# Kernel tuning notes

Measured on AMD Instinct MI355X. Metric: run time of the kernel, lower is better.

## Reference

```python
import jax, jax.numpy as jnp
import numpy as np

B, C, H, W = 8, 512, 96, 96
CQ = 64  # in_places // scale
EPS = 1e-06


def setup_inputs() -> dict:
    key = jax.random.key(0)
    ks = jax.random.split(key, 4)
    x = jax.random.normal(ks[0], (B, C, H, W), dtype=jnp.float32)
    wq = jax.random.normal(ks[1], (CQ, C), dtype=jnp.float32) * (1.0 / np.sqrt(C))
    wk = jax.random.normal(ks[2], (CQ, C), dtype=jnp.float32) * (1.0 / np.sqrt(C))
    wv = jax.random.normal(ks[3], (C, C), dtype=jnp.float32) * (1.0 / np.sqrt(C))
    bq = jnp.zeros((CQ,), jnp.float32)
    bk = jnp.zeros((CQ,), jnp.float32)
    bv = jnp.zeros((C,), jnp.float32)
    gamma = jnp.ones((1,), jnp.float32)
    return {"x": x, "wq": wq, "bq": bq, "wk": wk, "bk": bk, "wv": wv, "bv": bv, "gamma": gamma}


def reference(x, wq, bq, wk, bk, wv, bv, gamma):
    b, c, h, w = x.shape
    n = h * w
    xf = x.reshape(b, c, n)  # [b, c, n]
    # 1x1 convs == per-position channel GEMMs
    Q = jnp.einsum('oc,bcn->bon', wq, xf) + bq[None, :, None]  # [b, cq, n]
    K = jnp.einsum('oc,bcn->bon', wk, xf) + bk[None, :, None]  # [b, cq, n]
    V = jnp.einsum('oc,bcn->bon', wv, xf) + bv[None, :, None]  # [b, c, n]
    # L2 normalize over channel dim (dim=-2), matching torch l2_norm (no eps)
    Q = Q / jnp.linalg.norm(Q, axis=1, keepdims=True)
    K = K / jnp.linalg.norm(K, axis=1, keepdims=True)
    Qt = jnp.transpose(Q, (0, 2, 1))  # [b, n, cq]
    # tailor_sum = 1 / (N + Q . (sum_n K + eps))
    k_sum = K.sum(axis=-1) + EPS  # [b, cq]
    tailor = 1.0 / (n + jnp.einsum('bnm,bm->bn', Qt, k_sum))  # [b, n]
    v_sum = V.sum(axis=-1)  # [b, c]
    matrix = jnp.einsum('bmn,bcn->bmc', K, V)  # [b, cq, c]
    matrix_sum = v_sum[:, :, None] + jnp.einsum('bnm,bmc->bcn', Qt, matrix)  # [b, c, n]
    weight_value = matrix_sum * tailor[:, None, :]  # [b, c, n]
    return x + gamma[0] * weight_value.reshape(b, c, h, w)
```

## Files before the change

### kernel.cpp

```cpp
#include <hip/hip_runtime.h>

#define NB 8
#define NC 512
#define NQ 64
#define NN 9216
#define FEPS 1e-6f

typedef __attribute__((ext_vector_type(8))) short s16x8;
typedef __attribute__((ext_vector_type(4))) float f32x4;

static const size_t OFF_Q    = 0;
static const size_t OFF_KT   = OFF_Q + (size_t)NB * NQ * NN;
static const size_t OFF_KSUM = OFF_KT + (size_t)NB * NQ * NN;
static const size_t OFF_XSUM = OFF_KSUM + (size_t)NB * NQ;
static const size_t OFF_M1   = OFF_XSUM + (size_t)NB * NC;
static const size_t OFF_M2   = OFF_M1 + (size_t)NB * NQ * NC;
static const size_t OFF_VSUM = OFF_M2 + (size_t)NB * NQ * NC;
static const size_t OFF_WB   = OFF_VSUM + (size_t)NB * NC;

__device__ __forceinline__ void load_lds16(const void* g, void* l) {
    __builtin_amdgcn_global_load_lds((const __attribute__((address_space(1))) void*)g,
                                     (__attribute__((address_space(3))) void*)l, 16, 0, 0);
}

__device__ __forceinline__ unsigned cvt_pk_bf16(float lo, float hi) {
    unsigned r;
    asm("v_cvt_pk_bf16_f32 %0, %1, %2" : "=v"(r) : "v"(lo), "v"(hi));
    return r;
}

__device__ __forceinline__ unsigned short f2bf(float f) {
    union { float f; unsigned u; } a; a.f = f;
    unsigned r = a.u + 0x7FFFu + ((a.u >> 16) & 1u);
    return (unsigned short)(r >> 16);
}

__global__ void prep_w_kernel(const float* __restrict__ wq, const float* __restrict__ wk,
                              unsigned short* __restrict__ Wb) {
    const int idx = blockIdx.x * 256 + threadIdx.x;
#pragma unroll
    for (int k = 0; k < 4; ++k) {
        const int f4 = idx + k * 4096;
        const float* src = (f4 < 8192) ? wq : wk;
        const float4 v = *(const float4*)&src[(size_t)(f4 & 8191) * 4];
        uint2 u;
        u.x = cvt_pk_bf16(v.x, v.y);
        u.y = cvt_pk_bf16(v.z, v.w);
        *(uint2*)&Wb[(size_t)f4 * 4] = u;
    }
}

__launch_bounds__(256, 3)
__global__ void qk_mfma_kernel(const float* __restrict__ x,
                               const unsigned short* __restrict__ Wb,
                               const float* __restrict__ bq, const float* __restrict__ bk,
                               float* __restrict__ Qt, unsigned short* __restrict__ Ktb,
                               float* __restrict__ ksum) {
    __shared__ __align__(16) unsigned short WX[12672];
    __shared__ float ssqL[4][64];
    unsigned short* Ws = WX;
    unsigned short* Xs = WX + 8192;
    const int t = threadIdx.x;
    const int w = t >> 6, lane = t & 63;
    const int g = lane >> 4, i16 = lane & 15;
    const int b = blockIdx.y;
    const int n0 = blockIdx.x * 64;
    const int srow = (w << 3) + (lane >> 3);
    const int sslot = lane & 7;

    f32x4 acc[2][4];
#pragma unroll
    for (int rt = 0; rt < 2; ++rt)
#pragma unroll
        for (int ct = 0; ct < 4; ++ct) acc[rt][ct] = {0.f, 0.f, 0.f, 0.f};

#pragma unroll 1
    for (int kc = 0; kc < NC; kc += 64) {
#pragma unroll
        for (int q = 0; q < 4; ++q) {
            const int row = q * 32 + srow;
            load_lds16(Wb + (size_t)row * NC + kc + ((sslot ^ (row & 7)) << 3),
                       Ws + (q * 32 + (w << 3)) * 64);
        }
#pragma unroll
        for (int r = 0; r < 2; ++r) {
            const int idx = r * 256 + t;
            const int cp = idx >> 4;
            const int p4 = (idx & 15) << 2;
            const float* xp = &x[((size_t)b * NC + kc + 2 * cp) * NN + n0 + p4];
            const float4 v0 = *(const float4*)xp;
            const float4 v1 = *(const float4*)(xp + NN);
            const float* f0 = (const float*)&v0;
            const float* f1 = (const float*)&v1;
#pragma unroll
            for (int j = 0; j < 4; ++j) {
                const int pos = p4 + j;
                const unsigned u = cvt_pk_bf16(f0[j], f1[j]);
                *(unsigned*)&Xs[pos * 64 + ((2 * cp) ^ ((pos & 7) << 3))] = u;
            }
        }
        __syncthreads();
#pragma unroll
        for (int ks = 0; ks < 2; ++ks) {
            s16x8 af[2], bfr[4];
#pragma unroll
            for (int rt = 0; rt < 2; ++rt) {
                const int row = (w << 5) + (rt << 4) + i16;
                af[rt] = *(const s16x8*)&Ws[row * 64 + (((ks << 5) + (g << 3)) ^ ((row & 7) << 3))];
            }
#pragma unroll
            for (int ct = 0; ct < 4; ++ct) {
                const int row = (ct << 4) + i16;
                bfr[ct] = *(const s16x8*)&Xs[row * 64 + (((ks << 5) + (g << 3)) ^ ((row & 7) << 3))];
            }
#pragma unroll
            for (int rt = 0; rt < 2; ++rt)
#pragma unroll
                for (int ct = 0; ct < 4; ++ct)
                    acc[rt][ct] = __builtin_amdgcn_mfma_f32_16x16x32_bf16(af[rt], bfr[ct], acc[rt][ct], 0, 0, 0);
        }
        __syncthreads();
    }

    const bool isK = (w >= 2);
    const int obase = (w & 1) * 32;
    const float* bias = isK ? bk : bq;
    float bv[2][4];
#pragma unroll
    for (int rt = 0; rt < 2; ++rt)
#pragma unroll
        for (int reg = 0; reg < 4; ++reg)
            bv[rt][reg] = bias[obase + rt * 16 + 4 * g + reg];
#pragma unroll
    for (int rt = 0; rt < 2; ++rt)
#pragma unroll
        for (int ct = 0; ct < 4; ++ct)
#pragma unroll
            for (int reg = 0; reg < 4; ++reg) acc[rt][ct][reg] += bv[rt][reg];

    float sq[4];
#pragma unroll
    for (int ct = 0; ct < 4; ++ct) {
        float s = 0.f;
#pragma unroll
        for (int rt = 0; rt < 2; ++rt)
#pragma unroll
            for (int reg = 0; reg < 4; ++reg) s += acc[rt][ct][reg] * acc[rt][ct][reg];
        s += __shfl_xor(s, 16, 64);
        s += __shfl_xor(s, 32, 64);
        sq[ct] = s;
    }
    ssqL[w][lane] = sq[g];
    __syncthreads();
    const int pairw = (w >> 1) << 1;
    float inv[4];
#pragma unroll
    for (int ct = 0; ct < 4; ++ct) {
        const int p = ct * 16 + i16;
        inv[ct] = rsqrtf(ssqL[pairw][p] + ssqL[pairw + 1][p]);
    }
#pragma unroll
    for (int rt = 0; rt < 2; ++rt)
#pragma unroll
        for (int ct = 0; ct < 4; ++ct)
#pragma unroll
            for (int reg = 0; reg < 4; ++reg) acc[rt][ct][reg] *= inv[ct];

    float* epQ = (float*)WX;
    unsigned short* epK = WX + 8320;
    if (!isK) {
#pragma unroll
        for (int rt = 0; rt < 2; ++rt)
#pragma unroll
            for (int ct = 0; ct < 4; ++ct)
#pragma unroll
                for (int reg = 0; reg < 4; ++reg)
                    epQ[(ct * 16 + i16) * 65 + (w * 32 + rt * 16 + 4 * g + reg)] = acc[rt][ct][reg];
    } else {
#pragma unroll
        for (int rt = 0; rt < 2; ++rt)
#pragma unroll
            for (int reg = 0; reg < 4; ++reg) {
                float s = acc[rt][0][reg] + acc[rt][1][reg] + acc[rt][2][reg] + acc[rt][3][reg];
                s += __shfl_xor(s, 1, 64);
                s += __shfl_xor(s, 2, 64);
                s += __shfl_xor(s, 4, 64);
                s += __shfl_xor(s, 8, 64);
                if (i16 == 0) atomicAdd(&ksum[b * NQ + obase + rt * 16 + 4 * g + reg], s);
            }
#pragma unroll
        for (int rt = 0; rt < 2; ++rt)
#pragma unroll
            for (int ct = 0; ct < 4; ++ct)
#pragma unroll
                for (int reg = 0; reg < 4; ++reg)
                    epK[(obase + rt * 16 + 4 * g + reg) * 68 + ct * 16 + i16] = f2bf(acc[rt][ct][reg]);
    }
    __syncthreads();
#pragma unroll
    for (int r = 0; r < 4; ++r) {
        const int idx = r * 256 + t;
        const int o = idx >> 4, p4 = (idx & 15) * 4;
        float4 v;
        v.x = epQ[(p4 + 0) * 65 + o];
        v.y = epQ[(p4 + 1) * 65 + o];
        v.z = epQ[(p4 + 2) * 65 + o];
        v.w = epQ[(p4 + 3) * 65 + o];
        *(float4*)&Qt[((size_t)b * NQ + o) * NN + n0 + p4] = v;
    }
#pragma unroll
    for (int r = 0; r < 2; ++r) {
        const int idx = r * 256 + t;
        const int o = idx >> 3, s8 = (idx & 7) * 8;
        uint4 pk;
        unsigned short* up = (unsigned short*)&pk;
#pragma unroll
        for (int j = 0; j < 8; ++j) up[j] = epK[o * 68 + s8 + j];
        *(uint4*)&Ktb[((size_t)b * NQ + o) * NN + n0 + s8] = pk;
    }
}

__launch_bounds__(256, 4)
__global__ void kxt_mfma_kernel(const float* __restrict__ x, const unsigned short* __restrict__ Ktb,
                                float* __restrict__ mat1, float* __restrict__ xsum) {
    __shared__ __align__(16) unsigned short Ks[64 * 64];
    __shared__ __align__(16) unsigned short Xs[64 * 64];
    const int t = threadIdx.x;
    const int w = t >> 6, lane = t & 63;
    const int g = lane >> 4, i16 = lane & 15;
    const int nch = blockIdx.x, ct0 = blockIdx.y, b = blockIdx.z;
    const int c0 = ct0 * 64;
    const int pbeg = nch * 576;
    const int srow = (w << 3) + (lane >> 3);
    const int sslot = lane & 7;

    f32x4 acc[4];
#pragma unroll
    for (int ct = 0; ct < 4; ++ct) acc[ct] = {0.f, 0.f, 0.f, 0.f};
    float xs4[4] = {0.f, 0.f, 0.f, 0.f};

#pragma unroll 1
    for (int p0 = pbeg; p0 < pbeg + 576; p0 += 64) {
#pragma unroll
        for (int q = 0; q < 2; ++q) {
            const int row = q * 32 + srow;
            load_lds16(Ktb + ((size_t)b * NQ + row) * NN + p0 + ((sslot ^ (row & 7)) << 3),
                       Ks + (q * 32 + (w << 3)) * 64);
        }
#pragma unroll
        for (int r = 0; r < 4; ++r) {
            const int idx = r * 256 + t;
            const int c = idx >> 4, n4 = (idx & 15) << 2;
            const float4 v = *(const float4*)&x[((size_t)b * NC + c0 + c) * NN + p0 + n4];
            xs4[r] += (v.x + v.y) + (v.z + v.w);
            uint2 u;
            u.x = cvt_pk_bf16(v.x, v.y);
            u.y = cvt_pk_bf16(v.z, v.w);
            *(uint2*)&Xs[c * 64 + (n4 ^ ((c & 7) << 3))] = u;
        }
        __syncthreads();
#pragma unroll
        for (int ks = 0; ks < 2; ++ks) {
            s16x8 a8, b8[4];
            {
                const int row = (w << 4) + i16;
                a8 = *(const s16x8*)&Ks[row * 64 + (((ks << 5) + (g << 3)) ^ ((row & 7) << 3))];
            }
#pragma unroll
            for (int ct = 0; ct < 4; ++ct) {
                const int row = (ct << 4) + i16;
                b8[ct] = *(const s16x8*)&Xs[row * 64 + (((ks << 5) + (g << 3)) ^ ((row & 7) << 3))];
            }
#pragma unroll
            for (int ct = 0; ct < 4; ++ct)
                acc[ct] = __builtin_amdgcn_mfma_f32_16x16x32_bf16(a8, b8[ct], acc[ct], 0, 0, 0);
        }
        __syncthreads();
    }
    const int ob = (w << 4) + 4 * g;
#pragma unroll
    for (int ct = 0; ct < 4; ++ct)
#pragma unroll
        for (int reg = 0; reg < 4; ++reg)
            atomicAdd(&mat1[((size_t)b * NQ + ob + reg) * NC + c0 + (ct << 4) + i16], acc[ct][reg]);
#pragma unroll
    for (int r = 0; r < 4; ++r) {
        float s = xs4[r];
        s += __shfl_xor(s, 1, 64);
        s += __shfl_xor(s, 2, 64);
        s += __shfl_xor(s, 4, 64);
        s += __shfl_xor(s, 8, 64);
        if (i16 == 0) atomicAdd(&xsum[b * NC + c0 + r * 16 + (t >> 4)], s);
    }
}

__launch_bounds__(256)
__global__ void mat2_kernel(const float* __restrict__ wv, const float* __restrict__ bv,
                            const float* __restrict__ mat1, const float* __restrict__ ksum,
                            const float* __restrict__ xsum,
                            float* __restrict__ mat2, float* __restrict__ vsum) {
    __shared__ __align__(16) float m1s[64 * 68];
    __shared__ __align__(16) float wvs[64 * 68];
    const int t = threadIdx.x;
    const int tx = t & 15, ty = t >> 4;
    const int ct = blockIdx.x, b = blockIdx.y;
    const int co0 = ct * 64;
    if (t < 64) {
        const int co = co0 + t;
        float s = 0.f;
        for (int c = 0; c < NC; ++c) s += wv[(size_t)co * NC + c] * xsum[b * NC + c];
        vsum[b * NC + co] = s + (float)NN * bv[co];
    }
    float acc[4][4] = {{0.f}};
    for (int cc = 0; cc < NC; cc += 64) {
#pragma unroll 1
        for (int r = 0; r < 4; ++r) {
            const int idx = r * 256 + t;
            const int row = idx >> 4, a = (idx & 15) * 4;
            *(float4*)&m1s[row * 68 + a] = *(const float4*)&mat1[((size_t)b * NQ + row) * NC + cc + a];
            *(float4*)&wvs[row * 68 + a] = *(const float4*)&wv[(size_t)(co0 + row) * NC + cc + a];
        }
        __syncthreads();
#pragma unroll 8
        for (int c4 = 0; c4 < 16; ++c4) {
            float4 mr[4], wr[4];
#pragma unroll
            for (int jo = 0; jo < 4; ++jo) mr[jo] = *(const float4*)&m1s[(ty + 16 * jo) * 68 + c4 * 4];
#pragma unroll
            for (int jc = 0; jc < 4; ++jc) wr[jc] = *(const float4*)&wvs[(tx + 16 * jc) * 68 + c4 * 4];
#pragma unroll
            for (int jo = 0; jo < 4; ++jo)
#pragma unroll
                for (int jc = 0; jc < 4; ++jc)
                    acc[jo][jc] += mr[jo].x * wr[jc].x + mr[jo].y * wr[jc].y +
                                   mr[jo].z * wr[jc].z + mr[jo].w * wr[jc].w;
        }
        __syncthreads();
    }
#pragma unroll
    for (int jo = 0; jo < 4; ++jo) {
        const float ks = ksum[b * NQ + ty + 16 * jo];
#pragma unroll
        for (int jc = 0; jc < 4; ++jc) {
            const int co = co0 + tx + 16 * jc;
            mat2[((size_t)b * NQ + ty + 16 * jo) * NC + co] = acc[jo][jc] + ks * bv[co];
        }
    }
}

__launch_bounds__(256, 4)
__global__ void final_kernel(const float* __restrict__ x, const float* __restrict__ Qt,
                             const float* __restrict__ ksum, const float* __restrict__ mat2,
                             const float* __restrict__ vsum, const float* __restrict__ gamma,
                             float* __restrict__ out) {
    __shared__ __align__(16) float qs[64 * 64];
    __shared__ __align__(16) float m2s[64 * 68];
    __shared__ float vs[64];
    __shared__ float ksl[64];
    __shared__ float tl[64];
    const int t = threadIdx.x;
    const int a = t & 15, cq = t >> 4;
    const int wid = t >> 6, lane = t & 63;
    const int lrow = lane >> 4, lcol = (lane & 15) * 4;
    const int b = blockIdx.y;
    const int n0 = blockIdx.x * 64;
#pragma unroll
    for (int q = 0; q < 4; ++q) {
        const int o0 = q * 16 + wid * 4;
        load_lds16(Qt + ((size_t)b * NQ + o0 + lrow) * NN + n0 + lcol, &qs[o0 * 64]);
    }
    if (t < 64) ksl[t] = ksum[b * NQ + t] + FEPS;
    __syncthreads();
    if (t < 64) {
        float s = 0.f;
#pragma unroll 8
        for (int o = 0; o < 64; ++o) s += qs[o * 64 + t] * ksl[o];
        tl[t] = 1.0f / ((float)NN + s);
    }
    __syncthreads();
    const float g = gamma[0];
    const float4 tlr = *(const float4*)&tl[a * 4];
    for (int cc = 0; cc < NC; cc += 64) {
#pragma unroll 1
        for (int r = 0; r < 4; ++r) {
            const int idx = r * 256 + t;
            const int o = idx >> 4, a4 = (idx & 15) * 4;
            *(float4*)&m2s[o * 68 + a4] = *(const float4*)&mat2[((size_t)b * NQ + o) * NC + cc + a4];
        }
        if (t < 64) vs[t] = vsum[b * NC + cc + t];
        __syncthreads();
        float acc[4][4];
#pragma unroll
        for (int u = 0; u < 4; ++u)
#pragma unroll
            for (int e = 0; e < 4; ++e) acc[u][e] = 0.f;
#pragma unroll 8
        for (int o = 0; o < 64; ++o) {
            const float4 qv = *(const float4*)&qs[o * 64 + a * 4];
            const float m0 = m2s[o * 68 + cq];
            const float m1 = m2s[o * 68 + cq + 16];
            const float m2v = m2s[o * 68 + cq + 32];
            const float m3 = m2s[o * 68 + cq + 48];
            acc[0][0] += qv.x * m0; acc[0][1] += qv.y * m0; acc[0][2] += qv.z * m0; acc[0][3] += qv.w * m0;
            acc[1][0] += qv.x * m1; acc[1][1] += qv.y * m1; acc[1][2] += qv.z * m1; acc[1][3] += qv.w * m1;
            acc[2][0] += qv.x * m2v; acc[2][1] += qv.y * m2v; acc[2][2] += qv.z * m2v; acc[2][3] += qv.w * m2v;
            acc[3][0] += qv.x * m3; acc[3][1] += qv.y * m3; acc[3][2] += qv.z * m3; acc[3][3] += qv.w * m3;
        }
#pragma unroll
        for (int u = 0; u < 4; ++u) {
            const int c = cc + cq + 16 * u;
            const size_t gi = ((size_t)b * NC + c) * NN + n0 + a * 4;
            const float4 xv = *(const float4*)&x[gi];
            const float vsv = vs[cq + 16 * u];
            float4 ov;
            ov.x = xv.x + g * (vsv + acc[u][0]) * tlr.x;
            ov.y = xv.y + g * (vsv + acc[u][1]) * tlr.y;
            ov.z = xv.z + g * (vsv + acc[u][2]) * tlr.z;
            ov.w = xv.w + g * (vsv + acc[u][3]) * tlr.w;
            *(float4*)&out[gi] = ov;
        }
        __syncthreads();
    }
}

extern "C" void kernel_launch(void* const* d_in, const int* in_sizes, int n_in,
                              void* d_out, int out_size, void* d_ws, size_t ws_size,
                              hipStream_t stream) {
    (void)in_sizes; (void)n_in; (void)out_size; (void)ws_size;
    const float* x     = (const float*)d_in[0];
    const float* wq    = (const float*)d_in[1];
    const float* bq    = (const float*)d_in[2];
    const float* wk    = (const float*)d_in[3];
    const float* bk    = (const float*)d_in[4];
    const float* wv    = (const float*)d_in[5];
    const float* bv    = (const float*)d_in[6];
    const float* gamma = (const float*)d_in[7];
    float* out = (float*)d_out;
    float* ws  = (float*)d_ws;

    float* Qt            = ws + OFF_Q;
    unsigned short* Ktb  = (unsigned short*)(ws + OFF_KT);
    float* ksum          = ws + OFF_KSUM;
    float* xsum          = ws + OFF_XSUM;
    float* m1            = ws + OFF_M1;
    float* m2            = ws + OFF_M2;
    float* vsum          = ws + OFF_VSUM;
    unsigned short* Wb   = (unsigned short*)(ws + OFF_WB);

    hipMemsetAsync(ksum, 0, (size_t)(NB * NQ + NB * NC + NB * NQ * NC) * sizeof(float), stream);

    prep_w_kernel<<<dim3(16), 256, 0, stream>>>(wq, wk, Wb);
    qk_mfma_kernel<<<dim3(NN / 64, NB), 256, 0, stream>>>(x, Wb, bq, bk, Qt, Ktb, ksum);
    kxt_mfma_kernel<<<dim3(16, 8, NB), 256, 0, stream>>>(x, Ktb, m1, xsum);
    mat2_kernel<<<dim3(8, NB), 256, 0, stream>>>(wv, bv, m1, ksum, xsum, m2, vsum);
    final_kernel<<<dim3(NN / 64, NB), 256, 0, stream>>>(x, Qt, ksum, m2, vsum, gamma, out);
}
```

Measured before the change: 452.1 us.

## Use bf16 MFMA in final kernel with swizzled bf16 Q and transposed mat2

Q is now stored as bf16 in a position-major, XOR-swizzled layout, and mat2 is written as transposed, swizzled bf16. The final kernel then computes Q^T·mat2 with bf16 MFMA instructions instead of scalar FP32 FMAs, and double-buffers the mat2 tiles through LDS with global_load_lds. This targets the FP32 ALU cost of the final contraction and halves the traffic for Q, at the price of bf16 precision in Q, mat2 and the tailor denominator.

```diff
diff --git a/kernel.cpp b/kernel.cpp
--- a/kernel.cpp
+++ b/kernel.cpp
@@ -54,7 +54,7 @@
 __global__ void qk_mfma_kernel(const float* __restrict__ x,
                                const unsigned short* __restrict__ Wb,
                                const float* __restrict__ bq, const float* __restrict__ bk,
-                               float* __restrict__ Qt, unsigned short* __restrict__ Ktb,
+                               unsigned short* __restrict__ Qtb, unsigned short* __restrict__ Ktb,
                                float* __restrict__ ksum) {
     __shared__ __align__(16) unsigned short WX[12672];
     __shared__ float ssqL[4][64];
@@ -166,7 +166,7 @@
 #pragma unroll
             for (int reg = 0; reg < 4; ++reg) acc[rt][ct][reg] *= inv[ct];
 
-    float* epQ = (float*)WX;
+    unsigned short* epQb = WX;
     unsigned short* epK = WX + 8320;
     if (!isK) {
 #pragma unroll
@@ -174,8 +174,11 @@
 #pragma unroll
             for (int ct = 0; ct < 4; ++ct)
 #pragma unroll
-                for (int reg = 0; reg < 4; ++reg)
-                    epQ[(ct * 16 + i16) * 65 + (w * 32 + rt * 16 + 4 * g + reg)] = acc[rt][ct][reg];
+                for (int reg = 0; reg < 4; ++reg) {
+                    const int o = w * 32 + rt * 16 + 4 * g + reg;
+                    const int pos = ct * 16 + i16;
+                    epQb[pos * 64 + (o ^ ((pos & 7) << 3))] = f2bf(acc[rt][ct][reg]);
+                }
     } else {
 #pragma unroll
         for (int rt = 0; rt < 2; ++rt)
@@ -197,16 +200,14 @@
                     epK[(obase + rt * 16 + 4 * g + reg) * 68 + ct * 16 + i16] = f2bf(acc[rt][ct][reg]);
     }
     __syncthreads();
-#pragma unroll
-    for (int r = 0; r < 4; ++r) {
-        const int idx = r * 256 + t;
-        const int o = idx >> 4, p4 = (idx & 15) * 4;
-        float4 v;
-        v.x = epQ[(p4 + 0) * 65 + o];
-        v.y = epQ[(p4 + 1) * 65 + o];
-        v.z = epQ[(p4 + 2) * 65 + o];
-        v.w = epQ[(p4 + 3) * 65 + o];
-        *(float4*)&Qt[((size_t)b * NQ + o) * NN + n0 + p4] = v;
+    {
+        const size_t base = ((size_t)b * NN + n0) * 64;
+        const uint4* src = (const uint4*)epQb;
+#pragma unroll
+        for (int r = 0; r < 2; ++r) {
+            const int idx = r * 256 + t;
+            *(uint4*)&Qtb[base + (size_t)idx * 8] = src[idx];
+        }
     }
 #pragma unroll
     for (int r = 0; r < 2; ++r) {
@@ -298,7 +299,7 @@
 __global__ void mat2_kernel(const float* __restrict__ wv, const float* __restrict__ bv,
                             const float* __restrict__ mat1, const float* __restrict__ ksum,
                             const float* __restrict__ xsum,
-                            float* __restrict__ mat2, float* __restrict__ vsum) {
+                            unsigned short* __restrict__ m2bT, float* __restrict__ vsum) {
     __shared__ __align__(16) float m1s[64 * 68];
     __shared__ __align__(16) float wvs[64 * 68];
     const int t = threadIdx.x;
@@ -340,84 +341,102 @@
 #pragma unroll
     for (int jo = 0; jo < 4; ++jo) {
         const float ks = ksum[b * NQ + ty + 16 * jo];
+        const int o = ty + 16 * jo;
 #pragma unroll
         for (int jc = 0; jc < 4; ++jc) {
             const int co = co0 + tx + 16 * jc;
-            mat2[((size_t)b * NQ + ty + 16 * jo) * NC + co] = acc[jo][jc] + ks * bv[co];
+            m2bT[((size_t)b * NC + co) * NQ + (o ^ ((co & 7) << 3))] = f2bf(acc[jo][jc] + ks * bv[co]);
         }
     }
 }
 
 __launch_bounds__(256, 4)
-__global__ void final_kernel(const float* __restrict__ x, const float* __restrict__ Qt,
-                             const float* __restrict__ ksum, const float* __restrict__ mat2,
-                             const float* __restrict__ vsum, const float* __restrict__ gamma,
-                             float* __restrict__ out) {
-    __shared__ __align__(16) float qs[64 * 64];
-    __shared__ __align__(16) float m2s[64 * 68];
-    __shared__ float vs[64];
+__global__ void final_mfma_kernel(const float* __restrict__ x, const unsigned short* __restrict__ Qtb,
+                                  const float* __restrict__ ksum, const unsigned short* __restrict__ m2bT,
+                                  const float* __restrict__ vsum, const float* __restrict__ gamma,
+                                  float* __restrict__ out) {
+    __shared__ __align__(16) unsigned short Qs[64 * 64];
+    __shared__ __align__(16) unsigned short Ms[2][64 * 64];
+    __shared__ float vsall[512];
     __shared__ float ksl[64];
     __shared__ float tl[64];
     const int t = threadIdx.x;
-    const int a = t & 15, cq = t >> 4;
-    const int wid = t >> 6, lane = t & 63;
-    const int lrow = lane >> 4, lcol = (lane & 15) * 4;
+    const int w = t >> 6, lane = t & 63;
+    const int g = lane >> 4, i16 = lane & 15;
     const int b = blockIdx.y;
     const int n0 = blockIdx.x * 64;
-#pragma unroll
-    for (int q = 0; q < 4; ++q) {
-        const int o0 = q * 16 + wid * 4;
-        load_lds16(Qt + ((size_t)b * NQ + o0 + lrow) * NN + n0 + lcol, &qs[o0 * 64]);
-    }
+
+    const unsigned short* qg = Qtb + ((size_t)b * NN + n0) * 64;
+    const unsigned short* mg = m2bT + (size_t)b * NC * 64;
+#pragma unroll
+    for (int r = 0; r < 2; ++r) {
+        const int off = (w * 2 + r) * 512;
+        load_lds16(qg + off + lane * 8, Qs + off);
+        load_lds16(mg + off + lane * 8, &Ms[0][off]);
+    }
+    vsall[t] = vsum[b * NC + t];
+    vsall[256 + t] = vsum[b * NC + 256 + t];
     if (t < 64) ksl[t] = ksum[b * NQ + t] + FEPS;
     __syncthreads();
     if (t < 64) {
         float s = 0.f;
-#pragma unroll 8
-        for (int o = 0; o < 64; ++o) s += qs[o * 64 + t] * ksl[o];
-        tl[t] = 1.0f / ((float)NN + s);
-    }
-    __syncthreads();
-    const float g = gamma[0];
-    const float4 tlr = *(const float4*)&tl[a * 4];
-    for (int cc = 0; cc < NC; cc += 64) {
-#pragma unroll 1
-        for (int r = 0; r < 4; ++r) {
-            const int idx = r * 256 + t;
-            const int o = idx >> 4, a4 = (idx & 15) * 4;
-            *(float4*)&m2s[o * 68 + a4] = *(const float4*)&mat2[((size_t)b * NQ + o) * NC + cc + a4];
-        }
-        if (t < 64) vs[t] = vsum[b * NC + cc + t];
-        __syncthreads();
-        float acc[4][4];
-#pragma unroll
-        for (int u = 0; u < 4; ++u)
-#pragma unroll
-            for (int e = 0; e < 4; ++e) acc[u][e] = 0.f;
+        const int sw = (t & 7) << 3;
 #pragma unroll 8
         for (int o = 0; o < 64; ++o) {
-            const float4 qv = *(const float4*)&qs[o * 64 + a * 4];
-            const float m0 = m2s[o * 68 + cq];
-            const float m1 = m2s[o * 68 + cq + 16];
-            const float m2v = m2s[o * 68 + cq + 32];
-            const float m3 = m2s[o * 68 + cq + 48];
-            acc[0][0] += qv.x * m0; acc[0][1] += qv.y * m0; acc[0][2] += qv.z * m0; acc[0][3] += qv.w * m0;
-            acc[1][0] += qv.x * m1; acc[1][1] += qv.y * m1; acc[1][2] += qv.z * m1; acc[1][3] += qv.w * m1;
-            acc[2][0] += qv.x * m2v; acc[2][1] += qv.y * m2v; acc[2][2] += qv.z * m2v; acc[2][3] += qv.w * m2v;
-            acc[3][0] += qv.x * m3; acc[3][1] += qv.y * m3; acc[3][2] += qv.z * m3; acc[3][3] += qv.w * m3;
-        }
-#pragma unroll
-        for (int u = 0; u < 4; ++u) {
-            const int c = cc + cq + 16 * u;
-            const size_t gi = ((size_t)b * NC + c) * NN + n0 + a * 4;
-            const float4 xv = *(const float4*)&x[gi];
-            const float vsv = vs[cq + 16 * u];
+            union { unsigned u; float f; } cv;
+            cv.u = (unsigned)Qs[t * 64 + o] << 16;
+            s += cv.f * ksl[o ^ sw];
+        }
+        tl[t] = 1.0f / ((float)NN + s);
+    }
+    s16x8 af[4][2];
+#pragma unroll
+    for (int mt = 0; mt < 4; ++mt)
+#pragma unroll
+        for (int ks = 0; ks < 2; ++ks) {
+            const int row = mt * 16 + i16;
+            af[mt][ks] = *(const s16x8*)&Qs[row * 64 + (((ks << 5) + (g << 3)) ^ ((row & 7) << 3))];
+        }
+    const float gm = gamma[0];
+    const int c_local = w * 16 + i16;
+    __syncthreads();
+
+#pragma unroll 1
+    for (int cc8 = 0; cc8 < 8; ++cc8) {
+        if (cc8 < 7) {
+#pragma unroll
+            for (int r = 0; r < 2; ++r) {
+                const int off = (w * 2 + r) * 512;
+                load_lds16(mg + (cc8 + 1) * 4096 + off + lane * 8, &Ms[(cc8 + 1) & 1][off]);
+            }
+        }
+        const unsigned short* mbuf = Ms[cc8 & 1];
+        s16x8 b8[2];
+#pragma unroll
+        for (int ks = 0; ks < 2; ++ks)
+            b8[ks] = *(const s16x8*)&mbuf[c_local * 64 + (((ks << 5) + (g << 3)) ^ ((i16 & 7) << 3))];
+        f32x4 acc[4];
+#pragma unroll
+        for (int mt = 0; mt < 4; ++mt) acc[mt] = {0.f, 0.f, 0.f, 0.f};
+#pragma unroll
+        for (int ks = 0; ks < 2; ++ks)
+#pragma unroll
+            for (int mt = 0; mt < 4; ++mt)
+                acc[mt] = __builtin_amdgcn_mfma_f32_16x16x32_bf16(af[mt][ks], b8[ks], acc[mt], 0, 0, 0);
+        const int c = cc8 * 64 + c_local;
+        const float vsv = vsall[c];
+        const size_t rowbase = ((size_t)b * NC + c) * NN + n0;
+#pragma unroll
+        for (int mt = 0; mt < 4; ++mt) {
+            const int p = mt * 16 + 4 * g;
+            const float4 xv = *(const float4*)&x[rowbase + p];
+            const float4 t4 = *(const float4*)&tl[p];
             float4 ov;
-            ov.x = xv.x + g * (vsv + acc[u][0]) * tlr.x;
-            ov.y = xv.y + g * (vsv + acc[u][1]) * tlr.y;
-            ov.z = xv.z + g * (vsv + acc[u][2]) * tlr.z;
-            ov.w = xv.w + g * (vsv + acc[u][3]) * tlr.w;
-            *(float4*)&out[gi] = ov;
+            ov.x = xv.x + gm * (vsv + acc[mt][0]) * t4.x;
+            ov.y = xv.y + gm * (vsv + acc[mt][1]) * t4.y;
+            ov.z = xv.z + gm * (vsv + acc[mt][2]) * t4.z;
+            ov.w = xv.w + gm * (vsv + acc[mt][3]) * t4.w;
+            *(float4*)&out[rowbase + p] = ov;
         }
         __syncthreads();
     }
@@ -438,20 +457,20 @@
     float* out = (float*)d_out;
     float* ws  = (float*)d_ws;
 
-    float* Qt            = ws + OFF_Q;
+    unsigned short* Qtb  = (unsigned short*)(ws + OFF_Q);
     unsigned short* Ktb  = (unsigned short*)(ws + OFF_KT);
     float* ksum          = ws + OFF_KSUM;
     float* xsum          = ws + OFF_XSUM;
     float* m1            = ws + OFF_M1;
-    float* m2            = ws + OFF_M2;
+    unsigned short* m2b  = (unsigned short*)(ws + OFF_M2);
     float* vsum          = ws + OFF_VSUM;
     unsigned short* Wb   = (unsigned short*)(ws + OFF_WB);
 
     hipMemsetAsync(ksum, 0, (size_t)(NB * NQ + NB * NC + NB * NQ * NC) * sizeof(float), stream);
 
     prep_w_kernel<<<dim3(16), 256, 0, stream>>>(wq, wk, Wb);
-    qk_mfma_kernel<<<dim3(NN / 64, NB), 256, 0, stream>>>(x, Wb, bq, bk, Qt, Ktb, ksum);
+    qk_mfma_kernel<<<dim3(NN / 64, NB), 256, 0, stream>>>(x, Wb, bq, bk, Qtb, Ktb, ksum);
     kxt_mfma_kernel<<<dim3(16, 8, NB), 256, 0, stream>>>(x, Ktb, m1, xsum);
-    mat2_kernel<<<dim3(8, NB), 256, 0, stream>>>(wv, bv, m1, ksum, xsum, m2, vsum);
-    final_kernel<<<dim3(NN / 64, NB), 256, 0, stream>>>(x, Qt, ksum, m2, vsum, gamma, out);
-}
+    mat2_kernel<<<dim3(8, NB), 256, 0, stream>>>(wv, bv, m1, ksum, xsum, m2b, vsum);
+    final_mfma_kernel<<<dim3(NN / 64, NB), 256, 0, stream>>>(x, Qtb, ksum, m2b, vsum, gamma, out);
+}
```

Result: faster. 436.7 us (-3.4%).
